# Kernel optimization log

Hardware: AMD Instinct MI355X
Metric: run time of the kernel (lower is better)

Reference implementation:

```python
import jax, jax.numpy as jnp
import numpy as np

N, T, D = 8192, 256, 44
H = 8
NUM_GROUPS = 1024


def setup_inputs() -> dict:
    key = jax.random.key(0)
    ks = jax.random.split(key, 10)
    x = jax.random.normal(ks[0], (N, T, D), dtype=jnp.float32)
    # last valid timestep index per path (== path_length - 1, values in [0, T))
    last_idx = jax.random.randint(ks[1], (N,), 0, T, dtype=jnp.int32)
    # sorted group assignment, NUM_GROUPS ragged groups over N paths
    group_ids = jnp.sort(jax.random.randint(ks[2], (N,), 0, NUM_GROUPS, dtype=jnp.int32))
    s = 1.0 / np.sqrt(H)
    W_ih = jax.random.uniform(ks[3], (4 * H, D), minval=-s, maxval=s, dtype=jnp.float32)
    W_hh = jax.random.uniform(ks[4], (4 * H, H), minval=-s, maxval=s, dtype=jnp.float32)
    b_ih = jax.random.uniform(ks[5], (4 * H,), minval=-s, maxval=s, dtype=jnp.float32)
    b_hh = jax.random.uniform(ks[6], (4 * H,), minval=-s, maxval=s, dtype=jnp.float32)
    fc_W = jax.random.uniform(ks[7], (1, H), minval=-s, maxval=s, dtype=jnp.float32)
    fc_b = jax.random.uniform(ks[8], (1,), minval=-s, maxval=s, dtype=jnp.float32)
    return {"x": x, "W_ih": W_ih, "W_hh": W_hh, "b_ih": b_ih, "b_hh": b_hh,
            "fc_W": fc_W, "fc_b": fc_b, "last_idx": last_idx, "group_ids": group_ids}


def _lstm(x, W_ih, W_hh, b_ih, b_hh):
    # x: [N, T, D] -> hs: [T, N, H]; torch gate order: i, f, g, o
    n = x.shape[0]
    h = W_hh.shape[1]
    # precompute input contribution once (hoisted out of scan)
    xg = jnp.einsum('ntd,gd->ntg', x, W_ih) + (b_ih + b_hh)  # [N, T, 4H]

    def step(carry, xg_t):
        hh, cc = carry
        gates = xg_t + hh @ W_hh.T  # [N, 4H]
        i, f, g, o = jnp.split(gates, 4, axis=-1)
        cc = jax.nn.sigmoid(f) * cc + jax.nn.sigmoid(i) * jnp.tanh(g)
        hh = jax.nn.sigmoid(o) * jnp.tanh(cc)
        return (hh, cc), hh

    h0 = jnp.zeros((n, h), x.dtype)
    _, hs = jax.lax.scan(step, (h0, h0), jnp.swapaxes(xg, 0, 1))
    return hs  # [T, N, H]


def reference(x, W_ih, W_hh, b_ih, b_hh, fc_W, fc_b, last_idx, group_ids):
    hs = _lstm(x, W_ih, W_hh, b_ih, b_hh)            # [T, N, H]
    h_last = hs[last_idx, jnp.arange(x.shape[0])]    # gather last valid step -> [N, H]
    seg = jax.ops.segment_sum(h_last, group_ids, num_segments=NUM_GROUPS)  # [G, H]
    logits = seg @ fc_W.T + fc_b                     # [G, 1]
    probs = jax.nn.softmax(logits, axis=0)           # softmax over groups (dim=0)
    return probs.reshape(1, -1)                      # [1, G]
```

## Files before the change

### kernel.cpp

```cpp
#include <hip/hip_runtime.h>

#define N_PATHS 8192
#define T_STEPS 256
#define D_IN    44
#define H_SZ    8
#define G4      32
#define NGROUPS 1024
#define TC      16


__device__ __forceinline__ float sigm_f(float x) {
    return __builtin_amdgcn_rcpf(1.0f + __expf(-x));
}
__device__ __forceinline__ float tanh_f(float x) {
    return 1.0f - 2.0f * __builtin_amdgcn_rcpf(1.0f + __expf(2.0f * x));
}

__global__ void prep_kernel(const float* __restrict__ W_ih, const float* __restrict__ b_ih,
                            const float* __restrict__ b_hh, const int* __restrict__ last_idx,
                            float* __restrict__ Wt, float* __restrict__ bias,
                            int* __restrict__ perm) {
    __shared__ int hist[256];
    __shared__ int off[256];
    const int tid = threadIdx.x;
    hist[tid] = 0;
    for (int idx = tid; idx < G4 * D_IN; idx += 256) {
        int g = idx / D_IN, d = idx - g * D_IN;
        int gp = ((g & 7) << 2) | (g >> 3);
        Wt[d * G4 + gp] = W_ih[idx];
    }
    if (tid < G4) {
        int gp = ((tid & 7) << 2) | (tid >> 3);
        bias[gp] = b_ih[tid] + b_hh[tid];
    }
    __syncthreads();
    for (int k = 0; k < N_PATHS / 256; ++k)
        atomicAdd(&hist[last_idx[k * 256 + tid]], 1);
    __syncthreads();
    if (tid == 0) {
        int run = 0;
        for (int i = 0; i < 256; ++i) { off[i] = run; run += hist[i]; }
    }
    __syncthreads();
    for (int k = 0; k < N_PATHS / 256; ++k) {
        int p = k * 256 + tid;
        int b = last_idx[p];
        int pos = atomicAdd(&off[b], 1);
        perm[pos] = p;
    }
}

__global__ __launch_bounds__(64, 1)
void lstm_kernel(const float* __restrict__ x, const float* __restrict__ Whh,
                 const float* __restrict__ Wt, const float* __restrict__ bias,
                 const float* __restrict__ fcW, const int* __restrict__ last_idx,
                 const int* __restrict__ perm, float* __restrict__ sout) {
    __shared__ float xg2[TC][160];
    __shared__ __align__(16) float hbuf[4][12];
    __shared__ __align__(16) float wtl[D_IN * G4];
    __shared__ __align__(16) float biasl[G4];

    const int lane = threadIdx.x;
    const int b = (N_PATHS / 4 - 1) - blockIdx.x;

    const int p0 = perm[4 * b + 0], p1 = perm[4 * b + 1];
    const int p2 = perm[4 * b + 2], p3 = perm[4 * b + 3];
    const int l0 = last_idx[p0], l1 = last_idx[p1];
    const int l2 = last_idx[p2], l3 = last_idx[p3];
    const int wmax = max(max(l0, l1), max(l2, l3));

    {
        const float4* wsrc = (const float4*)Wt;
#pragma unroll
        for (int k = 0; k < 6; ++k) {
            int idx = k * 64 + lane;
            if (idx < (D_IN * G4) / 4) *(float4*)&wtl[4 * idx] = wsrc[idx];
        }
        if (lane < G4 / 4) *(float4*)&biasl[4 * lane] = ((const float4*)bias)[lane];
    }

    const int pl1 = lane & 3, tc1 = lane >> 2;
    const int pl2 = lane >> 3, j = lane & 7;
    const bool act2 = lane < 32;

    const int pg1 = pl1 == 0 ? p0 : pl1 == 1 ? p1 : pl1 == 2 ? p2 : p3;
    const int pg2 = pl2 == 0 ? p0 : pl2 == 1 ? p1 : pl2 == 2 ? p2 : p3;
    const int lst2 = pl2 == 0 ? l0 : pl2 == 1 ? l1 : pl2 == 2 ? l2 : l3;

    float whh[4][8];
#pragma unroll
    for (int m = 0; m < 4; ++m) {
        const float4* r = (const float4*)(Whh + (m * 8 + j) * H_SZ);
        float4 a = r[0], c = r[1];
        whh[m][0] = a.x; whh[m][1] = a.y; whh[m][2] = a.z; whh[m][3] = a.w;
        whh[m][4] = c.x; whh[m][5] = c.y; whh[m][6] = c.z; whh[m][7] = c.w;
    }
    const float fcWj = fcW[j];

    float hval = 0.f, cval = 0.f, hlast = 0.f;
    if (act2) hbuf[pl2][j] = 0.f;

    const float* xrow_base = x + (size_t)pg1 * (T_STEPS * D_IN);
    const int nch = (wmax >> 4) + 1;

    float4 xv[11];
    {
        const float4* xr = (const float4*)(xrow_base + tc1 * D_IN);
#pragma unroll
        for (int q = 0; q < 11; ++q) xv[q] = xr[q];
    }

    for (int ch = 0; ch < nch; ++ch) {
        {
            float acc[32];
#pragma unroll
            for (int gq = 0; gq < 8; ++gq) {
                const float4 bv = *(const float4*)&biasl[4 * gq];
                acc[4 * gq + 0] = bv.x; acc[4 * gq + 1] = bv.y;
                acc[4 * gq + 2] = bv.z; acc[4 * gq + 3] = bv.w;
            }
#pragma unroll
            for (int q = 0; q < 11; ++q) {
                float4 v = xv[q];
#pragma unroll
                for (int r = 0; r < 4; ++r) {
                    const float xd = (r == 0) ? v.x : (r == 1) ? v.y : (r == 2) ? v.z : v.w;
                    const int d = 4 * q + r;
#pragma unroll
                    for (int gq = 0; gq < 8; ++gq) {
                        const float4 w = *(const float4*)&wtl[d * G4 + 4 * gq];
                        acc[4 * gq + 0] = fmaf(w.x, xd, acc[4 * gq + 0]);
                        acc[4 * gq + 1] = fmaf(w.y, xd, acc[4 * gq + 1]);
                        acc[4 * gq + 2] = fmaf(w.z, xd, acc[4 * gq + 2]);
                        acc[4 * gq + 3] = fmaf(w.w, xd, acc[4 * gq + 3]);
                    }
                    __builtin_amdgcn_sched_barrier(0);
                }
            }
#pragma unroll
            for (int k = 0; k < 8; ++k) {
                float4 v = make_float4(acc[4 * k], acc[4 * k + 1], acc[4 * k + 2], acc[4 * k + 3]);
                *(float4*)&xg2[tc1][pl1 * 40 + 4 * k] = v;
            }
        }
        if (ch + 1 < nch) {
            const float4* xr = (const float4*)(xrow_base + ((ch + 1) * TC + tc1) * D_IN);
#pragma unroll
            for (int q = 0; q < 11; ++q) xv[q] = xr[q];
        }
        if (act2) {
            const int t0 = ch * TC;
#pragma unroll
            for (int tt = 0; tt < TC; ++tt) {
                const float4 xg = *(const float4*)&xg2[tt][pl2 * 40 + 4 * j];
                const float4 h01 = *(const float4*)&hbuf[pl2][0];
                const float4 h23 = *(const float4*)&hbuf[pl2][4];
                const float xgc[4] = {xg.x, xg.y, xg.z, xg.w};
                float pre[4];
#pragma unroll
                for (int m = 0; m < 4; ++m) {
                    float p = xgc[m];
                    p = fmaf(whh[m][0], h01.x, p); p = fmaf(whh[m][1], h01.y, p);
                    p = fmaf(whh[m][2], h01.z, p); p = fmaf(whh[m][3], h01.w, p);
                    p = fmaf(whh[m][4], h23.x, p); p = fmaf(whh[m][5], h23.y, p);
                    p = fmaf(whh[m][6], h23.z, p); p = fmaf(whh[m][7], h23.w, p);
                    pre[m] = p;
                }
                const float ig = sigm_f(pre[0]);
                const float fg = sigm_f(pre[1]);
                const float gg = tanh_f(pre[2]);
                const float og = sigm_f(pre[3]);
                cval = fmaf(fg, cval, ig * gg);
                hval = og * tanh_f(cval);
                const int t = t0 + tt;
                hlast = (t == lst2) ? hval : hlast;
                hbuf[pl2][j] = hval;
            }
        }
    }

    if (act2) {
        float v = hlast * fcWj;
        v += __shfl_xor(v, 1);
        v += __shfl_xor(v, 2);
        v += __shfl_xor(v, 4);
        if (j == 0) sout[pg2] = v;
    }
}

__global__ void finalize_kernel(const float* __restrict__ s, const int* __restrict__ gid,
                                float* __restrict__ out) {
    __shared__ float seg[NGROUPS];
    __shared__ float red[16];
    const int tid = threadIdx.x;
    seg[tid] = 0.f;
    __syncthreads();
#pragma unroll
    for (int k = 0; k < 8; ++k) {
        const int p = k * 1024 + tid;
        atomicAdd(&seg[gid[p]], s[p]);
    }
    __syncthreads();
    const float v = seg[tid];
    const int wid = tid >> 6, ln = tid & 63;
    float m = v;
#pragma unroll
    for (int o = 32; o >= 1; o >>= 1) m = fmaxf(m, __shfl_xor(m, o));
    if (ln == 0) red[wid] = m;
    __syncthreads();
    if (tid < 16) {
        float mm = red[tid];
#pragma unroll
        for (int o = 8; o >= 1; o >>= 1) mm = fmaxf(mm, __shfl_xor(mm, o));
        red[tid] = mm;
    }
    __syncthreads();
    const float vmax = red[0];
    __syncthreads();
    const float e = __expf(v - vmax);
    float ss = e;
#pragma unroll
    for (int o = 32; o >= 1; o >>= 1) ss += __shfl_xor(ss, o);
    if (ln == 0) red[wid] = ss;
    __syncthreads();
    if (tid < 16) {
        float s2 = red[tid];
#pragma unroll
        for (int o = 8; o >= 1; o >>= 1) s2 += __shfl_xor(s2, o);
        red[tid] = s2;
    }
    __syncthreads();
    const float tot = red[0];
    out[tid] = e / tot;
}

extern "C" void kernel_launch(void* const* d_in, const int* in_sizes, int n_in,
                              void* d_out, int out_size, void* d_ws, size_t ws_size,
                              hipStream_t stream) {
    const float* x      = (const float*)d_in[0];
    const float* W_ih   = (const float*)d_in[1];
    const float* W_hh   = (const float*)d_in[2];
    const float* b_ih   = (const float*)d_in[3];
    const float* b_hh   = (const float*)d_in[4];
    const float* fcW    = (const float*)d_in[5];
    const int* last_idx = (const int*)d_in[7];
    const int* gid      = (const int*)d_in[8];

    float* wsf  = (float*)d_ws;
    float* Wt   = wsf;
    float* bias = wsf + 1408;
    int*   perm = (int*)(wsf + 1440);
    float* sarr = wsf + 1440 + 8192;
    float* out  = (float*)d_out;

    hipLaunchKernelGGL(prep_kernel, dim3(1), dim3(256), 0, stream,
                       W_ih, b_ih, b_hh, last_idx, Wt, bias, perm);
    hipLaunchKernelGGL(lstm_kernel, dim3(N_PATHS / 4), dim3(64), 0, stream,
                       x, W_hh, Wt, bias, fcW, last_idx, perm, sarr);
    hipLaunchKernelGGL(finalize_kernel, dim3(1), dim3(1024), 0, stream,
                       sarr, gid, out);
}
```

Measured before the change: 543.4 us.

## Split LSTM block into producer and consumer waves with double-buffered gate staging

The LSTM block grows from one wave to two. Wave 0 computes the input projection for each 16-step chunk into a double-buffered shared array. Wave 1 runs the serial recurrence on the previous chunk, with one block barrier per chunk handing buffers over. Before, a single wave ran the projection and the latency-bound recurrence one after the other; this lets them overlap. The cost is a barrier per chunk, twice the staging memory, and a changed launch-bounds hint that may affect register allocation and occupancy.

New measurement: 535.9 us. No clear change (-1.4%).

```diff
diff --git a/kernel.cpp b/kernel.cpp
--- a/kernel.cpp
+++ b/kernel.cpp
@@ -50,17 +50,19 @@
     }
 }
 
-__global__ __launch_bounds__(64, 1)
+__global__ __launch_bounds__(128, 2)
 void lstm_kernel(const float* __restrict__ x, const float* __restrict__ Whh,
                  const float* __restrict__ Wt, const float* __restrict__ bias,
                  const float* __restrict__ fcW, const int* __restrict__ last_idx,
                  const int* __restrict__ perm, float* __restrict__ sout) {
-    __shared__ float xg2[TC][160];
+    __shared__ float xg2[2][TC][160];
     __shared__ __align__(16) float hbuf[4][12];
     __shared__ __align__(16) float wtl[D_IN * G4];
     __shared__ __align__(16) float biasl[G4];
 
-    const int lane = threadIdx.x;
+    const int tid = threadIdx.x;
+    const int lane = tid & 63;
+    const int w = tid >> 6;
     const int b = (N_PATHS / 4 - 1) - blockIdx.x;
 
     const int p0 = perm[4 * b + 0], p1 = perm[4 * b + 1];
@@ -68,50 +70,32 @@
     const int l0 = last_idx[p0], l1 = last_idx[p1];
     const int l2 = last_idx[p2], l3 = last_idx[p3];
     const int wmax = max(max(l0, l1), max(l2, l3));
+    const int nch = (wmax >> 4) + 1;
 
     {
         const float4* wsrc = (const float4*)Wt;
 #pragma unroll
-        for (int k = 0; k < 6; ++k) {
-            int idx = k * 64 + lane;
+        for (int k = 0; k < 3; ++k) {
+            int idx = k * 128 + tid;
             if (idx < (D_IN * G4) / 4) *(float4*)&wtl[4 * idx] = wsrc[idx];
         }
-        if (lane < G4 / 4) *(float4*)&biasl[4 * lane] = ((const float4*)bias)[lane];
-    }
-
-    const int pl1 = lane & 3, tc1 = lane >> 2;
-    const int pl2 = lane >> 3, j = lane & 7;
-    const bool act2 = lane < 32;
-
-    const int pg1 = pl1 == 0 ? p0 : pl1 == 1 ? p1 : pl1 == 2 ? p2 : p3;
-    const int pg2 = pl2 == 0 ? p0 : pl2 == 1 ? p1 : pl2 == 2 ? p2 : p3;
-    const int lst2 = pl2 == 0 ? l0 : pl2 == 1 ? l1 : pl2 == 2 ? l2 : l3;
-
-    float whh[4][8];
-#pragma unroll
-    for (int m = 0; m < 4; ++m) {
-        const float4* r = (const float4*)(Whh + (m * 8 + j) * H_SZ);
-        float4 a = r[0], c = r[1];
-        whh[m][0] = a.x; whh[m][1] = a.y; whh[m][2] = a.z; whh[m][3] = a.w;
-        whh[m][4] = c.x; whh[m][5] = c.y; whh[m][6] = c.z; whh[m][7] = c.w;
-    }
-    const float fcWj = fcW[j];
-
-    float hval = 0.f, cval = 0.f, hlast = 0.f;
-    if (act2) hbuf[pl2][j] = 0.f;
-
-    const float* xrow_base = x + (size_t)pg1 * (T_STEPS * D_IN);
-    const int nch = (wmax >> 4) + 1;
-
-    float4 xv[11];
-    {
-        const float4* xr = (const float4*)(xrow_base + tc1 * D_IN);
-#pragma unroll
-        for (int q = 0; q < 11; ++q) xv[q] = xr[q];
-    }
-
-    for (int ch = 0; ch < nch; ++ch) {
+        if (tid < G4 / 4) *(float4*)&biasl[4 * tid] = ((const float4*)bias)[tid];
+    }
+    __syncthreads();
+
+    if (w == 0) {
+        const int pl1 = lane & 3, tc1 = lane >> 2;
+        const int pg1 = pl1 == 0 ? p0 : pl1 == 1 ? p1 : pl1 == 2 ? p2 : p3;
+        const float* xrow_base = x + (size_t)pg1 * (T_STEPS * D_IN);
+
+        float4 xv[11];
         {
+            const float4* xr = (const float4*)(xrow_base + tc1 * D_IN);
+#pragma unroll
+            for (int q = 0; q < 11; ++q) xv[q] = xr[q];
+        }
+
+        for (int ch = 0; ch < nch; ++ch) {
             float acc[32];
 #pragma unroll
             for (int gq = 0; gq < 8; ++gq) {
@@ -128,11 +112,11 @@
                     const int d = 4 * q + r;
 #pragma unroll
                     for (int gq = 0; gq < 8; ++gq) {
-                        const float4 w = *(const float4*)&wtl[d * G4 + 4 * gq];
-                        acc[4 * gq + 0] = fmaf(w.x, xd, acc[4 * gq + 0]);
-                        acc[4 * gq + 1] = fmaf(w.y, xd, acc[4 * gq + 1]);
-                        acc[4 * gq + 2] = fmaf(w.z, xd, acc[4 * gq + 2]);
-                        acc[4 * gq + 3] = fmaf(w.w, xd, acc[4 * gq + 3]);
+                        const float4 ww = *(const float4*)&wtl[d * G4 + 4 * gq];
+                        acc[4 * gq + 0] = fmaf(ww.x, xd, acc[4 * gq + 0]);
+                        acc[4 * gq + 1] = fmaf(ww.y, xd, acc[4 * gq + 1]);
+                        acc[4 * gq + 2] = fmaf(ww.z, xd, acc[4 * gq + 2]);
+                        acc[4 * gq + 3] = fmaf(ww.w, xd, acc[4 * gq + 3]);
                     }
                     __builtin_amdgcn_sched_barrier(0);
                 }
@@ -140,51 +124,74 @@
 #pragma unroll
             for (int k = 0; k < 8; ++k) {
                 float4 v = make_float4(acc[4 * k], acc[4 * k + 1], acc[4 * k + 2], acc[4 * k + 3]);
-                *(float4*)&xg2[tc1][pl1 * 40 + 4 * k] = v;
-            }
-        }
-        if (ch + 1 < nch) {
-            const float4* xr = (const float4*)(xrow_base + ((ch + 1) * TC + tc1) * D_IN);
-#pragma unroll
-            for (int q = 0; q < 11; ++q) xv[q] = xr[q];
-        }
+                *(float4*)&xg2[ch & 1][tc1][pl1 * 40 + 4 * k] = v;
+            }
+            if (ch + 1 < nch) {
+                const float4* xr = (const float4*)(xrow_base + ((ch + 1) * TC + tc1) * D_IN);
+#pragma unroll
+                for (int q = 0; q < 11; ++q) xv[q] = xr[q];
+            }
+            __syncthreads();
+        }
+    } else {
+        const int pl2 = lane >> 3, j = lane & 7;
+        const bool act2 = lane < 32;
+        const int pg2 = pl2 == 0 ? p0 : pl2 == 1 ? p1 : pl2 == 2 ? p2 : p3;
+        const int lst2 = pl2 == 0 ? l0 : pl2 == 1 ? l1 : pl2 == 2 ? l2 : l3;
+
+        float whh[4][8];
+#pragma unroll
+        for (int m = 0; m < 4; ++m) {
+            const float4* r = (const float4*)(Whh + (m * 8 + j) * H_SZ);
+            float4 a = r[0], c = r[1];
+            whh[m][0] = a.x; whh[m][1] = a.y; whh[m][2] = a.z; whh[m][3] = a.w;
+            whh[m][4] = c.x; whh[m][5] = c.y; whh[m][6] = c.z; whh[m][7] = c.w;
+        }
+        const float fcWj = fcW[j];
+
+        float hval = 0.f, cval = 0.f, hlast = 0.f;
+        if (act2) hbuf[pl2][j] = 0.f;
+
+        for (int ch = 0; ch < nch; ++ch) {
+            __syncthreads();
+            if (act2) {
+                const int t0 = ch * TC;
+#pragma unroll
+                for (int tt = 0; tt < TC; ++tt) {
+                    const float4 xg = *(const float4*)&xg2[ch & 1][tt][pl2 * 40 + 4 * j];
+                    const float4 h01 = *(const float4*)&hbuf[pl2][0];
+                    const float4 h23 = *(const float4*)&hbuf[pl2][4];
+                    const float xgc[4] = {xg.x, xg.y, xg.z, xg.w};
+                    float pre[4];
+#pragma unroll
+                    for (int m = 0; m < 4; ++m) {
+                        float p = xgc[m];
+                        p = fmaf(whh[m][0], h01.x, p); p = fmaf(whh[m][1], h01.y, p);
+                        p = fmaf(whh[m][2], h01.z, p); p = fmaf(whh[m][3], h01.w, p);
+                        p = fmaf(whh[m][4], h23.x, p); p = fmaf(whh[m][5], h23.y, p);
+                        p = fmaf(whh[m][6], h23.z, p); p = fmaf(whh[m][7], h23.w, p);
+                        pre[m] = p;
+                    }
+                    const float ig = sigm_f(pre[0]);
+                    const float fg = sigm_f(pre[1]);
+                    const float gg = tanh_f(pre[2]);
+                    const float og = sigm_f(pre[3]);
+                    cval = fmaf(fg, cval, ig * gg);
+                    hval = og * tanh_f(cval);
+                    const int t = t0 + tt;
+                    hlast = (t == lst2) ? hval : hlast;
+                    hbuf[pl2][j] = hval;
+                }
+            }
+        }
+
         if (act2) {
-            const int t0 = ch * TC;
-#pragma unroll
-            for (int tt = 0; tt < TC; ++tt) {
-                const float4 xg = *(const float4*)&xg2[tt][pl2 * 40 + 4 * j];
-                const float4 h01 = *(const float4*)&hbuf[pl2][0];
-                const float4 h23 = *(const float4*)&hbuf[pl2][4];
-                const float xgc[4] = {xg.x, xg.y, xg.z, xg.w};
-                float pre[4];
-#pragma unroll
-                for (int m = 0; m < 4; ++m) {
-                    float p = xgc[m];
-                    p = fmaf(whh[m][0], h01.x, p); p = fmaf(whh[m][1], h01.y, p);
-                    p = fmaf(whh[m][2], h01.z, p); p = fmaf(whh[m][3], h01.w, p);
-                    p = fmaf(whh[m][4], h23.x, p); p = fmaf(whh[m][5], h23.y, p);
-                    p = fmaf(whh[m][6], h23.z, p); p = fmaf(whh[m][7], h23.w, p);
-                    pre[m] = p;
-                }
-                const float ig = sigm_f(pre[0]);
-                const float fg = sigm_f(pre[1]);
-                const float gg = tanh_f(pre[2]);
-                const float og = sigm_f(pre[3]);
-                cval = fmaf(fg, cval, ig * gg);
-                hval = og * tanh_f(cval);
-                const int t = t0 + tt;
-                hlast = (t == lst2) ? hval : hlast;
-                hbuf[pl2][j] = hval;
-            }
-        }
-    }
-
-    if (act2) {
-        float v = hlast * fcWj;
-        v += __shfl_xor(v, 1);
-        v += __shfl_xor(v, 2);
-        v += __shfl_xor(v, 4);
-        if (j == 0) sout[pg2] = v;
+            float v = hlast * fcWj;
+            v += __shfl_xor(v, 1);
+            v += __shfl_xor(v, 2);
+            v += __shfl_xor(v, 4);
+            if (j == 0) sout[pg2] = v;
+        }
     }
 }
 
@@ -255,7 +262,7 @@
 
     hipLaunchKernelGGL(prep_kernel, dim3(1), dim3(256), 0, stream,
                        W_ih, b_ih, b_hh, last_idx, Wt, bias, perm);
-    hipLaunchKernelGGL(lstm_kernel, dim3(N_PATHS / 4), dim3(64), 0, stream,
+    hipLaunchKernelGGL(lstm_kernel, dim3(N_PATHS / 4), dim3(128), 0, stream,
                        x, W_hh, Wt, bias, fcW, last_idx, perm, sarr);
     hipLaunchKernelGGL(finalize_kernel, dim3(1), dim3(1024), 0, stream,
                        sarr, gid, out);
```
